# Optimization experiments

Measured on AMD Instinct MI355X. Metric: run time of the kernel, lower is better.

The kernel has to match this reference:

```python
import jax, jax.numpy as jnp
import numpy as np

EPS = 1e-5  # nn.InstanceNorm2d default eps


def bilinear_warp(source, flow):
    """Faithful port of util.bilinear_warp: base grid in [-1,1] (align_corners=True
    convention, /(w-1)), flow normalized by 2/w, 2/h, then bilinear grid_sample
    with zero padding for out-of-bounds samples.
    source: [b,c,h,w], flow: [b,2,h,w] (pixel displacements)."""
    b, c, h, w = source.shape
    dt = source.dtype
    xs = jnp.arange(w, dtype=dt) / (w - 1)          # [w]
    ys = jnp.arange(h, dtype=dt) / (h - 1)          # [h]
    sx = (2.0 * xs - 1.0)[None, None, :] + 2.0 * flow[:, 0] / w   # [b,h,w]
    sy = (2.0 * ys - 1.0)[None, :, None] + 2.0 * flow[:, 1] / h   # [b,h,w]
    # normalized [-1,1] -> pixel coords (align_corners=True)
    ix = (sx + 1.0) * 0.5 * (w - 1)
    iy = (sy + 1.0) * 0.5 * (h - 1)
    x0 = jnp.floor(ix)
    y0 = jnp.floor(iy)
    wx1 = ix - x0
    wy1 = iy - y0

    def gather(yy, xx):
        valid = ((xx >= 0) & (xx <= w - 1) & (yy >= 0) & (yy <= h - 1)).astype(dt)
        xi = jnp.clip(xx, 0, w - 1).astype(jnp.int32)
        yi = jnp.clip(yy, 0, h - 1).astype(jnp.int32)
        # per-batch gather: [b,c,h,w]
        v = jax.vmap(lambda s, yb, xb: s[:, yb, xb])(source, yi, xi)
        return v * valid[:, None, :, :]

    out = ((1 - wy1) * (1 - wx1))[:, None] * gather(y0, x0) \
        + ((1 - wy1) * wx1)[:, None] * gather(y0, x0 + 1) \
        + (wy1 * (1 - wx1))[:, None] * gather(y0 + 1, x0) \
        + (wy1 * wx1)[:, None] * gather(y0 + 1, x0 + 1)
    return out


def instance_norm(x):
    # InstanceNorm2d(affine=False): per (b,c) biased stats over H,W
    mean = x.mean(axis=(2, 3), keepdims=True)
    var = x.var(axis=(2, 3), keepdims=True)
    return (x - mean) * jax.lax.rsqrt(var + EPS)


def setup_inputs() -> dict:
    key = jax.random.key(0)
    k1, k2, k3, k4, k5 = jax.random.split(key, 5)
    B, C, H, W = 4, 128, 256, 256
    return {
        "h": jax.random.normal(k1, (B, C, H, W), dtype=jnp.float32),
        "gamma": jax.random.normal(k2, (B, C, H, W), dtype=jnp.float32),
        "beta": jax.random.normal(k3, (B, C, H, W), dtype=jnp.float32),
        "flow": jax.random.normal(k4, (B, 2, H, W), dtype=jnp.float32),
        "flow_mask": jax.random.uniform(k5, (B, 1, H, W), dtype=jnp.float32),
    }


def reference(h, gamma, beta, flow, flow_mask):
    h_norm = instance_norm(h)
    gamma_w = bilinear_warp(gamma, flow)
    beta_w = bilinear_warp(beta, flow)
    return (gamma_w * flow_mask + h * (1.0 - flow_mask)) * h_norm + beta_w
```

## Files before the change

### kernel.cpp

```cpp
#include <hip/hip_runtime.h>

constexpr int Bx = 4;
constexpr int Cx = 128;
constexpr int Hx = 256;
constexpr int Wx = 256;
constexpr int HWx = Hx * Wx;

__global__ __launch_bounds__(512) void in_stats(const float* __restrict__ h,
                                                float* __restrict__ stats) {
    const int g = blockIdx.x;
    const int t = threadIdx.x;
    const float4* p = reinterpret_cast<const float4*>(h + (size_t)g * HWx);

    float4 s4 = {0.f, 0.f, 0.f, 0.f};
    float4 q4 = {0.f, 0.f, 0.f, 0.f};
    for (int i = t; i < HWx / 4; i += 512) {
        float4 v = p[i];
        s4.x += v.x; s4.y += v.y; s4.z += v.z; s4.w += v.w;
        q4.x += v.x * v.x; q4.y += v.y * v.y;
        q4.z += v.z * v.z; q4.w += v.w * v.w;
    }
    float s = (s4.x + s4.y) + (s4.z + s4.w);
    float q = (q4.x + q4.y) + (q4.z + q4.w);

    for (int off = 32; off > 0; off >>= 1) {
        s += __shfl_down(s, off, 64);
        q += __shfl_down(q, off, 64);
    }
    __shared__ float rs[8], rq[8];
    const int wid = t >> 6;
    if ((t & 63) == 0) { rs[wid] = s; rq[wid] = q; }
    __syncthreads();
    if (t == 0) {
        float S = 0.f, Q = 0.f;
        #pragma unroll
        for (int i = 0; i < 8; ++i) { S += rs[i]; Q += rq[i]; }
        const float mean = S * (1.0f / HWx);
        const float var  = Q * (1.0f / HWx) - mean * mean;
        stats[g]           = mean;
        stats[Bx * Cx + g] = rsqrtf(var + 1e-5f);
    }
}

__global__ __launch_bounds__(256) void fuse_kernel(
    const float* __restrict__ h,
    const float* __restrict__ gamma,
    const float* __restrict__ beta,
    const float* __restrict__ flow,
    const float* __restrict__ mask,
    const float* __restrict__ stats,
    float* __restrict__ out)
{
    const int p = blockIdx.x * 256 + threadIdx.x;
    const int b   = p >> 16;
    const int pix = p & (HWx - 1);
    const int y   = pix >> 8;
    const int x   = pix & (Wx - 1);

    const float fx = flow[(size_t)b * 2 * HWx + pix];
    const float fy = flow[(size_t)b * 2 * HWx + HWx + pix];
    const float m  = mask[(size_t)b * HWx + pix];

    const float xs = (float)x / 255.0f;
    const float ys = (float)y / 255.0f;
    const float sx = 2.0f * xs - 1.0f + 2.0f * fx / 256.0f;
    const float sy = 2.0f * ys - 1.0f + 2.0f * fy / 256.0f;
    const float ix = (sx + 1.0f) * 0.5f * 255.0f;
    const float iy = (sy + 1.0f) * 0.5f * 255.0f;

    const float x0f = floorf(ix);
    const float y0f = floorf(iy);
    const float wx1 = ix - x0f;
    const float wy1 = iy - y0f;
    const int x0 = (int)x0f, y0 = (int)y0f;
    const int x1 = x0 + 1,  y1 = y0 + 1;

    const bool vx0 = (x0 >= 0) & (x0 <= Wx - 1);
    const bool vx1 = (x1 >= 0) & (x1 <= Wx - 1);
    const bool vy0 = (y0 >= 0) & (y0 <= Hx - 1);
    const bool vy1 = (y1 >= 0) & (y1 <= Hx - 1);
    const int cx0 = min(max(x0, 0), Wx - 1), cx1 = min(max(x1, 0), Wx - 1);
    const int cy0 = min(max(y0, 0), Hx - 1), cy1 = min(max(y1, 0), Hx - 1);

    const float w00 = (1.0f - wy1) * (1.0f - wx1) * ((vy0 & vx0) ? 1.f : 0.f);
    const float w01 = (1.0f - wy1) * wx1          * ((vy0 & vx1) ? 1.f : 0.f);
    const float w10 = wy1 * (1.0f - wx1)          * ((vy1 & vx0) ? 1.f : 0.f);
    const float w11 = wy1 * wx1                   * ((vy1 & vx1) ? 1.f : 0.f);

    const int o00 = cy0 * Wx + cx0, o01 = cy0 * Wx + cx1;
    const int o10 = cy1 * Wx + cx0, o11 = cy1 * Wx + cx1;

    const size_t bbase = (size_t)b * Cx * HWx;
    const float* __restrict__ gb = gamma + bbase;
    const float* __restrict__ bb = beta  + bbase;
    const float* __restrict__ hb = h     + bbase + pix;
    float* __restrict__       ob = out   + bbase + pix;
    const float* __restrict__ meanp = stats + b * Cx;
    const float* __restrict__ isp   = stats + Bx * Cx + b * Cx;

    #pragma unroll 8
    for (int c = 0; c < Cx; ++c) {
        const size_t coff = (size_t)c * HWx;
        const float gw = w00 * gb[coff + o00] + w01 * gb[coff + o01]
                       + w10 * gb[coff + o10] + w11 * gb[coff + o11];
        const float bw = w00 * bb[coff + o00] + w01 * bb[coff + o01]
                       + w10 * bb[coff + o10] + w11 * bb[coff + o11];
        const float hv = hb[coff];
        const float hn = (hv - meanp[c]) * isp[c];
        ob[coff] = (gw * m + hv * (1.0f - m)) * hn + bw;
    }
}

extern "C" void kernel_launch(void* const* d_in, const int* in_sizes, int n_in,
                              void* d_out, int out_size, void* d_ws, size_t ws_size,
                              hipStream_t stream) {
    const float* h     = (const float*)d_in[0];
    const float* gamma = (const float*)d_in[1];
    const float* beta  = (const float*)d_in[2];
    const float* flow  = (const float*)d_in[3];
    const float* mask  = (const float*)d_in[4];
    float* out   = (float*)d_out;
    float* stats = (float*)d_ws;

    in_stats<<<Bx * Cx, 512, 0, stream>>>(h, stats);
    fuse_kernel<<<(Bx * HWx) / 256, 256, 0, stream>>>(h, gamma, beta, flow, mask,
                                                      stats, out);
}
```

Measured before the change: 566.6 us.

## Split channel loop into chunks across workgroups with XCD-aware block swizzle

The fused kernel now splits the 128-channel loop into 8 chunks of 16, launching 8x more workgroups. Each workgroup covers one image row. Block indices are remapped so consecutive hardware blocks spread across chunks, likely to balance work across the XCDs. Stats are interleaved as (mean, inv-std) pairs and the stats loop gets an unroll pragma. This raises parallelism and memory-level concurrency, at the cost of recomputing the bilinear coordinates and weights once per chunk.

```diff
diff --git a/kernel.cpp b/kernel.cpp
--- a/kernel.cpp
+++ b/kernel.cpp
@@ -5,6 +5,8 @@
 constexpr int Hx = 256;
 constexpr int Wx = 256;
 constexpr int HWx = Hx * Wx;
+constexpr int NCHUNK = 8;
+constexpr int CPT = Cx / NCHUNK;
 
 __global__ __launch_bounds__(512) void in_stats(const float* __restrict__ h,
                                                 float* __restrict__ stats) {
@@ -14,6 +16,7 @@
 
     float4 s4 = {0.f, 0.f, 0.f, 0.f};
     float4 q4 = {0.f, 0.f, 0.f, 0.f};
+    #pragma unroll 4
     for (int i = t; i < HWx / 4; i += 512) {
         float4 v = p[i];
         s4.x += v.x; s4.y += v.y; s4.z += v.z; s4.w += v.w;
@@ -37,8 +40,8 @@
         for (int i = 0; i < 8; ++i) { S += rs[i]; Q += rq[i]; }
         const float mean = S * (1.0f / HWx);
         const float var  = Q * (1.0f / HWx) - mean * mean;
-        stats[g]           = mean;
-        stats[Bx * Cx + g] = rsqrtf(var + 1e-5f);
+        stats[2 * g]     = mean;
+        stats[2 * g + 1] = rsqrtf(var + 1e-5f);
     }
 }
 
@@ -51,11 +54,16 @@
     const float* __restrict__ stats,
     float* __restrict__ out)
 {
-    const int p = blockIdx.x * 256 + threadIdx.x;
-    const int b   = p >> 16;
-    const int pix = p & (HWx - 1);
-    const int y   = pix >> 8;
-    const int x   = pix & (Wx - 1);
+    constexpr int NWG = NCHUNK * Bx * Hx;
+    const int orig = blockIdx.x;
+    const int bid  = (orig & 7) * (NWG / 8) + (orig >> 3);
+
+    const int chunk = bid >> 10;
+    const int rem   = bid & 1023;
+    const int b     = rem >> 8;
+    const int y     = rem & (Hx - 1);
+    const int x     = threadIdx.x;
+    const int pix   = (y << 8) | x;
 
     const float fx = flow[(size_t)b * 2 * HWx + pix];
     const float fy = flow[(size_t)b * 2 * HWx + HWx + pix];
@@ -90,23 +98,23 @@
     const int o00 = cy0 * Wx + cx0, o01 = cy0 * Wx + cx1;
     const int o10 = cy1 * Wx + cx0, o11 = cy1 * Wx + cx1;
 
-    const size_t bbase = (size_t)b * Cx * HWx;
-    const float* __restrict__ gb = gamma + bbase;
-    const float* __restrict__ bb = beta  + bbase;
-    const float* __restrict__ hb = h     + bbase + pix;
-    float* __restrict__       ob = out   + bbase + pix;
-    const float* __restrict__ meanp = stats + b * Cx;
-    const float* __restrict__ isp   = stats + Bx * Cx + b * Cx;
+    const int c0 = chunk * CPT;
+    const size_t cbase = (size_t)(b * Cx + c0) * HWx;
+    const float* __restrict__ gb = gamma + cbase;
+    const float* __restrict__ bb = beta  + cbase;
+    const float* __restrict__ hb = h     + cbase + pix;
+    float* __restrict__       ob = out   + cbase + pix;
+    const float* __restrict__ stp = stats + 2 * (b * Cx + c0);
 
-    #pragma unroll 8
-    for (int c = 0; c < Cx; ++c) {
+    #pragma unroll 4
+    for (int c = 0; c < CPT; ++c) {
         const size_t coff = (size_t)c * HWx;
         const float gw = w00 * gb[coff + o00] + w01 * gb[coff + o01]
                        + w10 * gb[coff + o10] + w11 * gb[coff + o11];
         const float bw = w00 * bb[coff + o00] + w01 * bb[coff + o01]
                        + w10 * bb[coff + o10] + w11 * bb[coff + o11];
         const float hv = hb[coff];
-        const float hn = (hv - meanp[c]) * isp[c];
+        const float hn = (hv - stp[2 * c]) * stp[2 * c + 1];
         ob[coff] = (gw * m + hv * (1.0f - m)) * hn + bw;
     }
 }
@@ -123,6 +131,6 @@
     float* stats = (float*)d_ws;
 
     in_stats<<<Bx * Cx, 512, 0, stream>>>(h, stats);
-    fuse_kernel<<<(Bx * HWx) / 256, 256, 0, stream>>>(h, gamma, beta, flow, mask,
+    fuse_kernel<<<NCHUNK * Bx * Hx, 256, 0, stream>>>(h, gamma, beta, flow, mask,
                                                       stats, out);
 }
```

Result: no change. 566.0 us (-0.1%).
